# Kernel optimization log

Measured on AMD Instinct MI355X. Metric: run time of the kernel, lower is better.

Reference implementation:

```python
import jax, jax.numpy as jnp
import numpy as np

B, N, F = 32, 64, 128          # batch, num_nodes, n_in_node
K, H, M, NH = 4, 256, 256, 256 # edge_types, msg_hid, msg_out, n_hid
E = N * (N - 1)                # fully-connected directed edges = 4032


def setup_inputs() -> dict:
    key = jax.random.key(0)
    ks = jax.random.split(key, 12)
    inputs = jax.random.normal(ks[0], (B, N, F), dtype=jnp.float32)
    # soft edge-type assignment per edge (rows sum to 1, as in NRI)
    rel_type = jax.nn.softmax(jax.random.normal(ks[1], (B, E, K), dtype=jnp.float32), axis=-1)
    # one-hot receiver/sender matrices for all i != j pairs
    idx = np.array([(i, j) for i in range(N) for j in range(N) if i != j], dtype=np.int64)
    eye = np.eye(N, dtype=np.float32)
    rel_rec = jnp.asarray(eye[idx[:, 0]])   # [E, N]
    rel_send = jnp.asarray(eye[idx[:, 1]])  # [E, N]
    # per-edge-type message MLP weights (stacked over K): y = x @ W + b
    W1 = jax.random.normal(ks[2], (K, 2 * F, H), dtype=jnp.float32) / np.sqrt(2 * F)
    b1 = jnp.zeros((K, H), dtype=jnp.float32)
    W2 = jax.random.normal(ks[3], (K, H, M), dtype=jnp.float32) / np.sqrt(H)
    b2 = jnp.zeros((K, M), dtype=jnp.float32)
    # output MLP
    Wo1 = jax.random.normal(ks[4], (F + M, NH), dtype=jnp.float32) / np.sqrt(F + M)
    bo1 = jnp.zeros((NH,), dtype=jnp.float32)
    Wo2 = jax.random.normal(ks[5], (NH, NH), dtype=jnp.float32) / np.sqrt(NH)
    bo2 = jnp.zeros((NH,), dtype=jnp.float32)
    Wo3 = jax.random.normal(ks[6], (NH, F), dtype=jnp.float32) / np.sqrt(NH)
    bo3 = jnp.zeros((F,), dtype=jnp.float32)
    return {"inputs": inputs, "rel_type": rel_type, "rel_rec": rel_rec, "rel_send": rel_send,
            "W1": W1, "b1": b1, "W2": W2, "b2": b2,
            "Wo1": Wo1, "bo1": bo1, "Wo2": Wo2, "bo2": bo2, "Wo3": Wo3, "bo3": bo3}


def reference(inputs, rel_type, rel_rec, rel_send, W1, b1, W2, b2, Wo1, bo1, Wo2, bo2, Wo3, bo3):
    # gather node states to edges via one-hot matmul (as in the source)
    receivers = jnp.einsum('en,bnf->bef', rel_rec, inputs)   # [B,E,F]
    senders = jnp.einsum('en,bnf->bef', rel_send, inputs)    # [B,E,F]
    pre_msg = jnp.concatenate([receivers, senders], axis=-1)  # [B,E,2F]
    # per-edge-type 2-layer ReLU MLP, batched over the K edge types
    h = jax.nn.relu(jnp.einsum('bef,kfh->bkeh', pre_msg, W1) + b1[:, None, :])  # [B,K,E,H]
    msg = jax.nn.relu(jnp.einsum('bkeh,khm->bkem', h, W2) + b2[:, None, :])     # [B,K,E,M]
    # mask by soft edge type and accumulate over types (dropout p=0 -> identity)
    all_msgs = jnp.einsum('bkem,bek->bem', msg, rel_type)     # [B,E,M]
    # scatter-aggregate messages to receiver nodes via one-hot matmul
    agg_msgs = jnp.einsum('en,bem->bnm', rel_rec, all_msgs)   # [B,N,M]
    aug = jnp.concatenate([inputs, agg_msgs], axis=-1)        # [B,N,F+M]
    p = jax.nn.relu(aug @ Wo1 + bo1)
    p = jax.nn.relu(p @ Wo2 + bo2)
    p = p @ Wo3 + bo3
    return inputs + p
```

## Files before the change

### kernel.cpp

```cpp
#include <hip/hip_runtime.h>


#define B_ 32
#define N_ 64
#define F_ 128
#define K_ 4
#define E_ 4032

#define WS_W2T 0u
#define WS_R   524288u
#define WS_S   4718592u
#define WS_AGG 8912896u

typedef unsigned short u16;
typedef u16    u16x4  __attribute__((ext_vector_type(4)));
typedef u16    u16x8  __attribute__((ext_vector_type(8)));
typedef __bf16 bf16x8 __attribute__((ext_vector_type(8)));
typedef float  f32x4  __attribute__((ext_vector_type(4)));
typedef float  f32x16 __attribute__((ext_vector_type(16)));

__device__ __forceinline__ u16 f2bf(float f) {
    unsigned u; __builtin_memcpy(&u, &f, 4);
    return (u16)((u + 0x7FFFu + ((u >> 16) & 1u)) >> 16);
}
__device__ __forceinline__ float bf2f(u16 u) {
    unsigned v = ((unsigned)u) << 16;
    float f; __builtin_memcpy(&f, &v, 4); return f;
}

#define LBAR() do { \
    asm volatile("s_waitcnt lgkmcnt(0)" ::: "memory"); \
    __builtin_amdgcn_s_barrier(); \
    __builtin_amdgcn_sched_barrier(0); \
} while (0)

__global__ __launch_bounds__(256) void prep_rs_kernel(
    const float* __restrict__ W2, const float* __restrict__ x,
    const float* __restrict__ W1, const float* __restrict__ b1,
    u16* __restrict__ W2t, u16* __restrict__ R, u16* __restrict__ S)
{
    __shared__ u16 ldsA[64 * 136];
    __shared__ u16 ldsW[32 * 136];
    const int tid = threadIdx.x;

    if (blockIdx.x < 1024) {
        unsigned gid = blockIdx.x * 256u + tid;
        unsigned n = gid & 255u, kk = (gid >> 8) & 255u, k = gid >> 16;
        unsigned dst = (k * 8u + (kk >> 5)) * 8192u
                     + ((((kk >> 4) & 1u) * 2u) + ((kk >> 3) & 1u)) * 2048u
                     + n * 8u + (kk & 7u);
        W2t[dst] = f2bf(W2[gid]);
        return;
    }

    const int lane = tid & 63, w = tid >> 6;
    const int quad = lane >> 4, mloc = lane & 15;
    const int bx = blockIdx.x - 1024;
    const int ch = bx & 1;
    const int bq = bx >> 1;
    const int k = bq >> 6, half = (bq >> 5) & 1, b = bq & 31;

    for (int idx = tid; idx < 2048; idx += 256) {
        int row = idx >> 5, c4 = idx & 31;
        f32x4 v = *(const f32x4*)&x[(b * 64 + row) * 128 + c4 * 4];
        u16x4 o;
#pragma unroll
        for (int e = 0; e < 4; ++e) o[e] = f2bf(v[e]);
        *(u16x4*)&ldsA[row * 136 + c4 * 4] = o;
    }
    __syncthreads();

    bf16x8 aF[4];
#pragma unroll
    for (int ks = 0; ks < 4; ++ks)
        aF[ks] = *(const bf16x8*)&ldsA[(w * 16 + mloc) * 136 + quad * 8 + ks * 32];

    u16* dst = half ? S : R;
    for (int c = ch * 4; c < ch * 4 + 4; ++c) {
        __syncthreads();
        for (int idx = tid; idx < 4096; idx += 256) {
            int n = idx & 31, f = idx >> 5;
            ldsW[n * 136 + f] = f2bf(W1[(k * 256 + half * 128 + f) * 256 + c * 32 + n]);
        }
        __syncthreads();
#pragma unroll
        for (int nt = 0; nt < 2; ++nt) {
            f32x4 acc = (f32x4){0.f, 0.f, 0.f, 0.f};
            const int boff = (nt * 16 + mloc) * 136 + quad * 8;
#pragma unroll
            for (int ks = 0; ks < 4; ++ks)
                acc = __builtin_amdgcn_mfma_f32_16x16x32_bf16(
                    aF[ks], *(const bf16x8*)&ldsW[boff + ks * 32], acc, 0, 0, 0);
            const int n = c * 32 + nt * 16 + mloc;
            const float bias = half ? 0.f : b1[k * 256 + n];
#pragma unroll
            for (int r = 0; r < 4; ++r) {
                int row = w * 16 + quad * 4 + r;
                if (half) {
                    dst[((size_t)((k * 8 + c) * 2048 + b * 64 + row)) * 32 + nt * 16 + mloc]
                        = f2bf(acc[r] + bias);
                } else {
                    dst[((size_t)(k * 2048 + b * 64 + row)) * 256 + n] = f2bf(acc[r] + bias);
                }
            }
        }
    }
}

__global__ __launch_bounds__(256, 3) void edge12_kernel(
    const u16* __restrict__ R, const u16* __restrict__ S2,
    const float* __restrict__ rel, const u16* __restrict__ W2t,
    const float* __restrict__ b2, u16* __restrict__ aggb)
{
    __shared__ u16   Hs[32][64][8];
    __shared__ float Rf[4][256];
    __shared__ float rtS[4][64];

    const int tid  = threadIdx.x;
    const int lane = tid & 63;
    const int w    = tid >> 6;
    const int l31  = lane & 31;
    const int lh   = lane >> 5;
    const int bid  = ((blockIdx.x & 7) << 8) | (blockIdx.x >> 3);
    const int b    = bid >> 6;
    const int i    = bid & 63;

    {
        const int k = tid >> 6, j = tid & 63;
        float v = 0.f;
        if (j != i) v = rel[((size_t)(b * E_) + i * 63 + (j - (j > i))) * 4 + k];
        rtS[k][j] = v;
    }
    {
        const int k = tid >> 6, e4 = tid & 63;
        u16x4 t4 = *(const u16x4*)&R[((size_t)(k * 2048 + b * 64 + i)) * 256 + e4 * 4];
#pragma unroll
        for (int e = 0; e < 4; ++e) Rf[k][e4 * 4 + e] = bf2f(t4[e]);
    }

    u16x8 sreg[8];
#pragma unroll
    for (int s = 0; s < 8; ++s)
        sreg[s] = *(const u16x8*)&S2[((size_t)(s * 2048 + b * 64 + lane)) * 32 + w * 8];

    __syncthreads();

    const u16* Wb = W2t + lh * 2048 + (w * 64 + l31) * 8;

    float amsg[2] = {0.f, 0.f};

    for (int kT = 0; kT < 4; ++kT) {
        bf16x8 Bb[2][2][2];
#pragma unroll
        for (int ks2 = 0; ks2 < 2; ++ks2) {
            const u16* wp = Wb + (size_t)(kT * 8) * 8192 + ks2 * 4096;
            Bb[0][ks2][0] = *(const bf16x8*)(wp);
            Bb[0][ks2][1] = *(const bf16x8*)(wp + 256);
        }
#pragma unroll
        for (int s = 0; s < 8; ++s) {
            const float* rp = &Rf[kT][s * 32 + w * 8];
            f32x4 r0 = *(const f32x4*)rp, r1 = *(const f32x4*)(rp + 4);
            bf16x8 o;
#pragma unroll
            for (int e = 0; e < 4; ++e) {
                o[e]     = (__bf16)fmaxf(r0[e] + bf2f(sreg[s][e]),     0.f);
                o[4 + e] = (__bf16)fmaxf(r1[e] + bf2f(sreg[s][4 + e]), 0.f);
            }
            *(bf16x8*)&Hs[s * 4 + w][lane][0] = o;
        }
        __syncthreads();

        f32x16 acc[2][2];
#pragma unroll
        for (int mt = 0; mt < 2; ++mt)
#pragma unroll
            for (int nt = 0; nt < 2; ++nt) acc[mt][nt] = (f32x16)(0.f);

#pragma unroll
        for (int kc = 0; kc < 8; ++kc) {
            const int cur = kc & 1, nxt = cur ^ 1;
            if (kc == 0 && kT < 3) {
#pragma unroll
                for (int s = 0; s < 8; ++s)
                    sreg[s] = *(const u16x8*)&S2[((size_t)(((kT + 1) * 8 + s) * 2048 + b * 64 + lane)) * 32 + w * 8];
            }
            if (kc < 7) {
#pragma unroll
                for (int ks2 = 0; ks2 < 2; ++ks2) {
                    const u16* wp = Wb + (size_t)(kT * 8 + kc + 1) * 8192 + ks2 * 4096;
                    Bb[nxt][ks2][0] = *(const bf16x8*)(wp);
                    Bb[nxt][ks2][1] = *(const bf16x8*)(wp + 256);
                }
            }
#pragma unroll
            for (int ks2 = 0; ks2 < 2; ++ks2) {
                const int g = kc * 4 + ks2 * 2 + lh;
                bf16x8 A0 = *(const bf16x8*)&Hs[g][l31][0];
                bf16x8 A1 = *(const bf16x8*)&Hs[g][32 + l31][0];
                acc[0][0] = __builtin_amdgcn_mfma_f32_32x32x16_bf16(A0, Bb[cur][ks2][0], acc[0][0], 0, 0, 0);
                acc[0][1] = __builtin_amdgcn_mfma_f32_32x32x16_bf16(A0, Bb[cur][ks2][1], acc[0][1], 0, 0, 0);
                acc[1][0] = __builtin_amdgcn_mfma_f32_32x32x16_bf16(A1, Bb[cur][ks2][0], acc[1][0], 0, 0, 0);
                acc[1][1] = __builtin_amdgcn_mfma_f32_32x32x16_bf16(A1, Bb[cur][ks2][1], acc[1][1], 0, 0, 0);
            }
        }

#pragma unroll
        for (int nt = 0; nt < 2; ++nt) {
            const float bias = b2[kT * 256 + w * 64 + nt * 32 + l31];
#pragma unroll
            for (int mt = 0; mt < 2; ++mt) {
                float s = 0.f;
#pragma unroll
                for (int rq = 0; rq < 4; ++rq) {
                    f32x4 rt4 = *(const f32x4*)&rtS[kT][mt * 32 + rq * 8 + 4 * lh];
#pragma unroll
                    for (int e = 0; e < 4; ++e) {
                        float v = acc[mt][nt][rq * 4 + e] + bias;
                        v = v > 0.f ? v : 0.f;
                        s += rt4[e] * v;
                    }
                }
                amsg[nt] += s;
            }
        }
        __syncthreads();
    }

#pragma unroll
    for (int nt = 0; nt < 2; ++nt) {
        float s = amsg[nt] + __shfl_xor(amsg[nt], 32);
        if (lh == 0)
            aggb[(size_t)(b * 64 + i) * 256 + w * 64 + nt * 32 + l31] = f2bf(s);
    }
}

__global__ __launch_bounds__(256) void outmlp5_kernel(
    const float* __restrict__ x, const u16* __restrict__ aggb,
    const float* __restrict__ Wo1, const float* __restrict__ bo1,
    const float* __restrict__ Wo2, const float* __restrict__ bo2,
    const float* __restrict__ Wo3, const float* __restrict__ bo3,
    float* __restrict__ out)
{
    __shared__ u16 p1S[16 * 264];
    __shared__ u16 p2S[16 * 264];
    const int tid = threadIdx.x, lane = tid & 63, w = tid >> 6;
    const int quad = lane >> 4, mloc = lane & 15;
    const int row0 = blockIdx.x * 16;

    {
        f32x4 acc[4];
#pragma unroll
        for (int nt = 0; nt < 4; ++nt) acc[nt] = (f32x4){0.f, 0.f, 0.f, 0.f};
        for (int kk = 0; kk < 12; ++kk) {
            bf16x8 aF;
            const int row = row0 + mloc;
            if (kk < 4) {
                u16x8 t;
#pragma unroll
                for (int e = 0; e < 8; ++e) t[e] = f2bf(x[row * 128 + kk * 32 + quad * 8 + e]);
                __builtin_memcpy(&aF, &t, 16);
            } else {
                aF = *(const bf16x8*)&aggb[(size_t)row * 256 + (kk - 4) * 32 + quad * 8];
            }
#pragma unroll
            for (int nt = 0; nt < 4; ++nt) {
                const int n = w * 64 + nt * 16 + mloc;
                u16x8 t;
#pragma unroll
                for (int e = 0; e < 8; ++e)
                    t[e] = f2bf(Wo1[(kk * 32 + quad * 8 + e) * 256 + n]);
                bf16x8 bF;
                __builtin_memcpy(&bF, &t, 16);
                acc[nt] = __builtin_amdgcn_mfma_f32_16x16x32_bf16(aF, bF, acc[nt], 0, 0, 0);
            }
        }
#pragma unroll
        for (int nt = 0; nt < 4; ++nt) {
            const int n = w * 64 + nt * 16 + mloc;
            const float bias = bo1[n];
#pragma unroll
            for (int r = 0; r < 4; ++r) {
                float v = acc[nt][r] + bias;
                p1S[(quad * 4 + r) * 264 + n] = f2bf(v > 0.f ? v : 0.f);
            }
        }
    }
    LBAR();
    {
        f32x4 acc[4];
#pragma unroll
        for (int nt = 0; nt < 4; ++nt) acc[nt] = (f32x4){0.f, 0.f, 0.f, 0.f};
        for (int kk = 0; kk < 8; ++kk) {
            bf16x8 aF = *(const bf16x8*)&p1S[mloc * 264 + kk * 32 + quad * 8];
#pragma unroll
            for (int nt = 0; nt < 4; ++nt) {
                const int n = w * 64 + nt * 16 + mloc;
                u16x8 t;
#pragma unroll
                for (int e = 0; e < 8; ++e)
                    t[e] = f2bf(Wo2[(kk * 32 + quad * 8 + e) * 256 + n]);
                bf16x8 bF;
                __builtin_memcpy(&bF, &t, 16);
                acc[nt] = __builtin_amdgcn_mfma_f32_16x16x32_bf16(aF, bF, acc[nt], 0, 0, 0);
            }
        }
#pragma unroll
        for (int nt = 0; nt < 4; ++nt) {
            const int n = w * 64 + nt * 16 + mloc;
            const float bias = bo2[n];
#pragma unroll
            for (int r = 0; r < 4; ++r) {
                float v = acc[nt][r] + bias;
                p2S[(quad * 4 + r) * 264 + n] = f2bf(v > 0.f ? v : 0.f);
            }
        }
    }
    LBAR();
    {
        f32x4 acc[2];
#pragma unroll
        for (int nt = 0; nt < 2; ++nt) acc[nt] = (f32x4){0.f, 0.f, 0.f, 0.f};
        for (int kk = 0; kk < 8; ++kk) {
            bf16x8 aF = *(const bf16x8*)&p2S[mloc * 264 + kk * 32 + quad * 8];
#pragma unroll
            for (int nt = 0; nt < 2; ++nt) {
                const int n = w * 32 + nt * 16 + mloc;
                u16x8 t;
#pragma unroll
                for (int e = 0; e < 8; ++e)
                    t[e] = f2bf(Wo3[(kk * 32 + quad * 8 + e) * 128 + n]);
                bf16x8 bF;
                __builtin_memcpy(&bF, &t, 16);
                acc[nt] = __builtin_amdgcn_mfma_f32_16x16x32_bf16(aF, bF, acc[nt], 0, 0, 0);
            }
        }
#pragma unroll
        for (int nt = 0; nt < 2; ++nt) {
            const int n = w * 32 + nt * 16 + mloc;
            const float bias = bo3[n];
#pragma unroll
            for (int r = 0; r < 4; ++r) {
                const int grow = row0 + quad * 4 + r;
                out[grow * 128 + n] = x[grow * 128 + n] + acc[nt][r] + bias;
            }
        }
    }
}

extern "C" void kernel_launch(void* const* d_in, const int* in_sizes, int n_in,
                              void* d_out, int out_size, void* d_ws, size_t ws_size,
                              hipStream_t stream) {
    const float* x   = (const float*)d_in[0];
    const float* rel = (const float*)d_in[1];
    const float* W1  = (const float*)d_in[4];
    const float* b1  = (const float*)d_in[5];
    const float* W2  = (const float*)d_in[6];
    const float* b2  = (const float*)d_in[7];
    const float* Wo1 = (const float*)d_in[8];
    const float* bo1 = (const float*)d_in[9];
    const float* Wo2 = (const float*)d_in[10];
    const float* bo2 = (const float*)d_in[11];
    const float* Wo3 = (const float*)d_in[12];
    const float* bo3 = (const float*)d_in[13];
    float* out = (float*)d_out;

    char* ws = (char*)d_ws;
    u16* W2t  = (u16*)(ws + WS_W2T);
    u16* R    = (u16*)(ws + WS_R);
    u16* S2   = (u16*)(ws + WS_S);
    u16* aggb = (u16*)(ws + WS_AGG);

    prep_rs_kernel<<<1536, 256, 0, stream>>>(W2, x, W1, b1, W2t, R, S2);
    edge12_kernel<<<2048, 256, 0, stream>>>(R, S2, rel, W2t, b2, aggb);
    outmlp5_kernel<<<128, 256, 0, stream>>>(x, aggb, Wo1, bo1, Wo2, bo2, Wo3, bo3, out);
}
```

Measured before the change: 193.3 us.

## Fuse three kernels into one persistent kernel with global atomic barriers

Replaces the three separate launches (prep, edge MLP, output MLP) with a single 512-block kernel that uses atomic-counter grid barriers between phases. Each block now processes four receiver nodes in the edge phase instead of one, and the prep work is redistributed across 512 blocks. The intent is to remove launch gaps and tail effects between kernels. In exchange it relies on all 512 blocks being co-resident for the spin barriers, adds a memset launch, and leaves most blocks idle in the final output-MLP phase.

```diff
diff --git a/kernel.cpp b/kernel.cpp
--- a/kernel.cpp
+++ b/kernel.cpp
@@ -11,6 +11,7 @@
 #define WS_R   524288u
 #define WS_S   4718592u
 #define WS_AGG 8912896u
+#define WS_BAR 9961472u
 
 typedef unsigned short u16;
 typedef u16    u16x4  __attribute__((ext_vector_type(4)));
@@ -34,315 +35,324 @@
     __builtin_amdgcn_sched_barrier(0); \
 } while (0)
 
-__global__ __launch_bounds__(256) void prep_rs_kernel(
-    const float* __restrict__ W2, const float* __restrict__ x,
-    const float* __restrict__ W1, const float* __restrict__ b1,
-    u16* __restrict__ W2t, u16* __restrict__ R, u16* __restrict__ S)
-{
-    __shared__ u16 ldsA[64 * 136];
-    __shared__ u16 ldsW[32 * 136];
-    const int tid = threadIdx.x;
-
-    if (blockIdx.x < 1024) {
-        unsigned gid = blockIdx.x * 256u + tid;
-        unsigned n = gid & 255u, kk = (gid >> 8) & 255u, k = gid >> 16;
-        unsigned dst = (k * 8u + (kk >> 5)) * 8192u
-                     + ((((kk >> 4) & 1u) * 2u) + ((kk >> 3) & 1u)) * 2048u
-                     + n * 8u + (kk & 7u);
-        W2t[dst] = f2bf(W2[gid]);
-        return;
-    }
-
-    const int lane = tid & 63, w = tid >> 6;
-    const int quad = lane >> 4, mloc = lane & 15;
-    const int bx = blockIdx.x - 1024;
-    const int ch = bx & 1;
-    const int bq = bx >> 1;
-    const int k = bq >> 6, half = (bq >> 5) & 1, b = bq & 31;
-
-    for (int idx = tid; idx < 2048; idx += 256) {
-        int row = idx >> 5, c4 = idx & 31;
-        f32x4 v = *(const f32x4*)&x[(b * 64 + row) * 128 + c4 * 4];
-        u16x4 o;
-#pragma unroll
-        for (int e = 0; e < 4; ++e) o[e] = f2bf(v[e]);
-        *(u16x4*)&ldsA[row * 136 + c4 * 4] = o;
+__device__ __forceinline__ void gbar(unsigned* c) {
+    __syncthreads();
+    if (threadIdx.x == 0) {
+        __threadfence();
+        atomicAdd(c, 1u);
+        int guard = 0;
+        while (atomicAdd(c, 0u) < 512u && guard < (1 << 22)) {
+            __builtin_amdgcn_s_sleep(8);
+            ++guard;
+        }
     }
     __syncthreads();
-
-    bf16x8 aF[4];
-#pragma unroll
-    for (int ks = 0; ks < 4; ++ks)
-        aF[ks] = *(const bf16x8*)&ldsA[(w * 16 + mloc) * 136 + quad * 8 + ks * 32];
-
-    u16* dst = half ? S : R;
-    for (int c = ch * 4; c < ch * 4 + 4; ++c) {
-        __syncthreads();
-        for (int idx = tid; idx < 4096; idx += 256) {
-            int n = idx & 31, f = idx >> 5;
-            ldsW[n * 136 + f] = f2bf(W1[(k * 256 + half * 128 + f) * 256 + c * 32 + n]);
-        }
-        __syncthreads();
-#pragma unroll
-        for (int nt = 0; nt < 2; ++nt) {
-            f32x4 acc = (f32x4){0.f, 0.f, 0.f, 0.f};
-            const int boff = (nt * 16 + mloc) * 136 + quad * 8;
-#pragma unroll
-            for (int ks = 0; ks < 4; ++ks)
-                acc = __builtin_amdgcn_mfma_f32_16x16x32_bf16(
-                    aF[ks], *(const bf16x8*)&ldsW[boff + ks * 32], acc, 0, 0, 0);
-            const int n = c * 32 + nt * 16 + mloc;
-            const float bias = half ? 0.f : b1[k * 256 + n];
-#pragma unroll
-            for (int r = 0; r < 4; ++r) {
-                int row = w * 16 + quad * 4 + r;
-                if (half) {
-                    dst[((size_t)((k * 8 + c) * 2048 + b * 64 + row)) * 32 + nt * 16 + mloc]
-                        = f2bf(acc[r] + bias);
-                } else {
-                    dst[((size_t)(k * 2048 + b * 64 + row)) * 256 + n] = f2bf(acc[r] + bias);
-                }
-            }
-        }
-    }
-}
-
-__global__ __launch_bounds__(256, 3) void edge12_kernel(
-    const u16* __restrict__ R, const u16* __restrict__ S2,
-    const float* __restrict__ rel, const u16* __restrict__ W2t,
-    const float* __restrict__ b2, u16* __restrict__ aggb)
+    __threadfence();
+}
+
+__global__ __launch_bounds__(256, 3) void fused_kernel(
+    const float* __restrict__ x, const float* __restrict__ rel,
+    const float* __restrict__ W1, const float* __restrict__ b1,
+    const float* __restrict__ W2, const float* __restrict__ b2,
+    const float* __restrict__ Wo1, const float* __restrict__ bo1,
+    const float* __restrict__ Wo2, const float* __restrict__ bo2,
+    const float* __restrict__ Wo3, const float* __restrict__ bo3,
+    u16* __restrict__ W2t, u16* __restrict__ R, u16* __restrict__ S2,
+    u16* __restrict__ aggb, float* __restrict__ out, unsigned* __restrict__ bar)
 {
-    __shared__ u16   Hs[32][64][8];
-    __shared__ float Rf[4][256];
-    __shared__ float rtS[4][64];
-
+    __shared__ __align__(16) char smem[37888];
     const int tid  = threadIdx.x;
     const int lane = tid & 63;
     const int w    = tid >> 6;
-    const int l31  = lane & 31;
-    const int lh   = lane >> 5;
-    const int bid  = ((blockIdx.x & 7) << 8) | (blockIdx.x >> 3);
-    const int b    = bid >> 6;
-    const int i    = bid & 63;
+    const int quad = lane >> 4, mloc = lane & 15;
+    const int l31  = lane & 31,  lh  = lane >> 5;
 
     {
-        const int k = tid >> 6, j = tid & 63;
-        float v = 0.f;
-        if (j != i) v = rel[((size_t)(b * E_) + i * 63 + (j - (j > i))) * 4 + k];
-        rtS[k][j] = v;
+        {
+            unsigned gbase = blockIdx.x * 512u + tid * 2u;
+#pragma unroll
+            for (int u2 = 0; u2 < 2; ++u2) {
+                unsigned gid = gbase + u2;
+                unsigned n = gid & 255u, kk = (gid >> 8) & 255u, k = gid >> 16;
+                unsigned dst = (k * 8u + (kk >> 5)) * 8192u
+                             + (((kk >> 4) & 1u) * 2u + ((kk >> 3) & 1u)) * 2048u
+                             + n * 8u + (kk & 7u);
+                W2t[dst] = f2bf(W2[gid]);
+            }
+        }
+        u16* ldsA = (u16*)smem;
+        u16* ldsW = (u16*)(smem + 17408);
+        const int bx = blockIdx.x;
+        const int k = bx >> 7, half = (bx >> 6) & 1, b = (bx >> 1) & 31, ch = bx & 1;
+
+        for (int idx = tid; idx < 2048; idx += 256) {
+            int row = idx >> 5, c4 = idx & 31;
+            f32x4 v = *(const f32x4*)&x[(b * 64 + row) * 128 + c4 * 4];
+            u16x4 o;
+#pragma unroll
+            for (int e = 0; e < 4; ++e) o[e] = f2bf(v[e]);
+            *(u16x4*)&ldsA[row * 136 + c4 * 4] = o;
+        }
+        __syncthreads();
+
+        bf16x8 aF[4];
+#pragma unroll
+        for (int ks = 0; ks < 4; ++ks)
+            aF[ks] = *(const bf16x8*)&ldsA[(w * 16 + mloc) * 136 + quad * 8 + ks * 32];
+
+        u16* dst = half ? S2 : R;
+        for (int c = ch * 4; c < ch * 4 + 4; ++c) {
+            __syncthreads();
+            for (int idx = tid; idx < 4096; idx += 256) {
+                int n = idx & 31, f = idx >> 5;
+                ldsW[n * 136 + f] = f2bf(W1[(k * 256 + half * 128 + f) * 256 + c * 32 + n]);
+            }
+            __syncthreads();
+#pragma unroll
+            for (int nt = 0; nt < 2; ++nt) {
+                f32x4 acc = (f32x4){0.f, 0.f, 0.f, 0.f};
+                const int boff = (nt * 16 + mloc) * 136 + quad * 8;
+#pragma unroll
+                for (int ks = 0; ks < 4; ++ks)
+                    acc = __builtin_amdgcn_mfma_f32_16x16x32_bf16(
+                        aF[ks], *(const bf16x8*)&ldsW[boff + ks * 32], acc, 0, 0, 0);
+                const int n = c * 32 + nt * 16 + mloc;
+                const float bias = half ? 0.f : b1[k * 256 + n];
+#pragma unroll
+                for (int r = 0; r < 4; ++r) {
+                    int row = w * 16 + quad * 4 + r;
+                    if (half) {
+                        dst[((size_t)((k * 8 + c) * 2048 + b * 64 + row)) * 32 + nt * 16 + mloc]
+                            = f2bf(acc[r] + bias);
+                    } else {
+                        dst[((size_t)(k * 2048 + b * 64 + row)) * 256 + n] = f2bf(acc[r] + bias);
+                    }
+                }
+            }
+        }
     }
+    gbar(&bar[0]);
+
     {
-        const int k = tid >> 6, e4 = tid & 63;
-        u16x4 t4 = *(const u16x4*)&R[((size_t)(k * 2048 + b * 64 + i)) * 256 + e4 * 4];
-#pragma unroll
-        for (int e = 0; e < 4; ++e) Rf[k][e4 * 4 + e] = bf2f(t4[e]);
+        u16  (*Hs)[64][8] = (u16(*)[64][8])smem;
+        float (*Rf)[256]  = (float(*)[256])(smem + 32768);
+        float (*rtS)[64]  = (float(*)[64])(smem + 32768 + 4096);
+        const int lbid = ((blockIdx.x & 7) << 6) | (blockIdx.x >> 3);
+        const int b    = lbid >> 4;
+        const int g    = lbid & 15;
+        const u16* Wb  = W2t + lh * 2048 + (w * 64 + l31) * 8;
+
+        for (int r = 0; r < 4; ++r) {
+            const int i = g * 4 + r;
+            {
+                const int k = tid >> 6, j = tid & 63;
+                float v = 0.f;
+                if (j != i) v = rel[((size_t)(b * E_) + i * 63 + (j - (j > i))) * 4 + k];
+                rtS[k][j] = v;
+            }
+            {
+                const int k = tid >> 6, e4 = tid & 63;
+                u16x4 t4 = *(const u16x4*)&R[((size_t)(k * 2048 + b * 64 + i)) * 256 + e4 * 4];
+#pragma unroll
+                for (int e = 0; e < 4; ++e) Rf[k][e4 * 4 + e] = bf2f(t4[e]);
+            }
+            u16x8 sreg[8];
+#pragma unroll
+            for (int s = 0; s < 8; ++s)
+                sreg[s] = *(const u16x8*)&S2[((size_t)(s * 2048 + b * 64 + lane)) * 32 + w * 8];
+            __syncthreads();
+
+            float amsg[2] = {0.f, 0.f};
+
+            for (int kT = 0; kT < 4; ++kT) {
+                bf16x8 Bb[2][2][2];
+#pragma unroll
+                for (int ks2 = 0; ks2 < 2; ++ks2) {
+                    const u16* wp = Wb + (size_t)(kT * 8) * 8192 + ks2 * 4096;
+                    Bb[0][ks2][0] = *(const bf16x8*)(wp);
+                    Bb[0][ks2][1] = *(const bf16x8*)(wp + 256);
+                }
+#pragma unroll
+                for (int s = 0; s < 8; ++s) {
+                    const float* rp = &Rf[kT][s * 32 + w * 8];
+                    f32x4 r0 = *(const f32x4*)rp, r1 = *(const f32x4*)(rp + 4);
+                    bf16x8 o;
+#pragma unroll
+                    for (int e = 0; e < 4; ++e) {
+                        o[e]     = (__bf16)fmaxf(r0[e] + bf2f(sreg[s][e]),     0.f);
+                        o[4 + e] = (__bf16)fmaxf(r1[e] + bf2f(sreg[s][4 + e]), 0.f);
+                    }
+                    *(bf16x8*)&Hs[s * 4 + w][lane][0] = o;
+                }
+                __syncthreads();
+
+                f32x16 acc[2][2];
+#pragma unroll
+                for (int mt = 0; mt < 2; ++mt)
+#pragma unroll
+                    for (int nt = 0; nt < 2; ++nt) acc[mt][nt] = (f32x16)(0.f);
+
+#pragma unroll
+                for (int kc = 0; kc < 8; ++kc) {
+                    const int cur = kc & 1, nxt = cur ^ 1;
+                    if (kc == 0 && kT < 3) {
+#pragma unroll
+                        for (int s = 0; s < 8; ++s)
+                            sreg[s] = *(const u16x8*)&S2[((size_t)(((kT + 1) * 8 + s) * 2048 + b * 64 + lane)) * 32 + w * 8];
+                    }
+                    if (kc < 7) {
+#pragma unroll
+                        for (int ks2 = 0; ks2 < 2; ++ks2) {
+                            const u16* wp = Wb + (size_t)(kT * 8 + kc + 1) * 8192 + ks2 * 4096;
+                            Bb[nxt][ks2][0] = *(const bf16x8*)(wp);
+                            Bb[nxt][ks2][1] = *(const bf16x8*)(wp + 256);
+                        }
+                    }
+#pragma unroll
+                    for (int ks2 = 0; ks2 < 2; ++ks2) {
+                        const int gg = kc * 4 + ks2 * 2 + lh;
+                        bf16x8 A0 = *(const bf16x8*)&Hs[gg][l31][0];
+                        bf16x8 A1 = *(const bf16x8*)&Hs[gg][32 + l31][0];
+                        acc[0][0] = __builtin_amdgcn_mfma_f32_32x32x16_bf16(A0, Bb[cur][ks2][0], acc[0][0], 0, 0, 0);
+                        acc[0][1] = __builtin_amdgcn_mfma_f32_32x32x16_bf16(A0, Bb[cur][ks2][1], acc[0][1], 0, 0, 0);
+                        acc[1][0] = __builtin_amdgcn_mfma_f32_32x32x16_bf16(A1, Bb[cur][ks2][0], acc[1][0], 0, 0, 0);
+                        acc[1][1] = __builtin_amdgcn_mfma_f32_32x32x16_bf16(A1, Bb[cur][ks2][1], acc[1][1], 0, 0, 0);
+                    }
+                }
+
+#pragma unroll
+                for (int nt = 0; nt < 2; ++nt) {
+                    const float bias = b2[kT * 256 + w * 64 + nt * 32 + l31];
+#pragma unroll
+                    for (int mt = 0; mt < 2; ++mt) {
+                        float s = 0.f;
+#pragma unroll
+                        for (int rq = 0; rq < 4; ++rq) {
+                            f32x4 rt4 = *(const f32x4*)&rtS[kT][mt * 32 + rq * 8 + 4 * lh];
+#pragma unroll
+                            for (int e = 0; e < 4; ++e) {
+                                float v = acc[mt][nt][rq * 4 + e] + bias;
+                                v = v > 0.f ? v : 0.f;
+                                s += rt4[e] * v;
+                            }
+                        }
+                        amsg[nt] += s;
+                    }
+                }
+                __syncthreads();
+            }
+
+#pragma unroll
+            for (int nt = 0; nt < 2; ++nt) {
+                float s = amsg[nt] + __shfl_xor(amsg[nt], 32);
+                if (lh == 0)
+                    aggb[(size_t)(b * 64 + i) * 256 + w * 64 + nt * 32 + l31] = f2bf(s);
+            }
+        }
     }
-
-    u16x8 sreg[8];
-#pragma unroll
-    for (int s = 0; s < 8; ++s)
-        sreg[s] = *(const u16x8*)&S2[((size_t)(s * 2048 + b * 64 + lane)) * 32 + w * 8];
-
-    __syncthreads();
-
-    const u16* Wb = W2t + lh * 2048 + (w * 64 + l31) * 8;
-
-    float amsg[2] = {0.f, 0.f};
-
-    for (int kT = 0; kT < 4; ++kT) {
-        bf16x8 Bb[2][2][2];
-#pragma unroll
-        for (int ks2 = 0; ks2 < 2; ++ks2) {
-            const u16* wp = Wb + (size_t)(kT * 8) * 8192 + ks2 * 4096;
-            Bb[0][ks2][0] = *(const bf16x8*)(wp);
-            Bb[0][ks2][1] = *(const bf16x8*)(wp + 256);
-        }
-#pragma unroll
-        for (int s = 0; s < 8; ++s) {
-            const float* rp = &Rf[kT][s * 32 + w * 8];
-            f32x4 r0 = *(const f32x4*)rp, r1 = *(const f32x4*)(rp + 4);
-            bf16x8 o;
-#pragma unroll
-            for (int e = 0; e < 4; ++e) {
-                o[e]     = (__bf16)fmaxf(r0[e] + bf2f(sreg[s][e]),     0.f);
-                o[4 + e] = (__bf16)fmaxf(r1[e] + bf2f(sreg[s][4 + e]), 0.f);
-            }
-            *(bf16x8*)&Hs[s * 4 + w][lane][0] = o;
-        }
-        __syncthreads();
-
-        f32x16 acc[2][2];
-#pragma unroll
-        for (int mt = 0; mt < 2; ++mt)
-#pragma unroll
-            for (int nt = 0; nt < 2; ++nt) acc[mt][nt] = (f32x16)(0.f);
-
-#pragma unroll
-        for (int kc = 0; kc < 8; ++kc) {
-            const int cur = kc & 1, nxt = cur ^ 1;
-            if (kc == 0 && kT < 3) {
-#pragma unroll
-                for (int s = 0; s < 8; ++s)
-                    sreg[s] = *(const u16x8*)&S2[((size_t)(((kT + 1) * 8 + s) * 2048 + b * 64 + lane)) * 32 + w * 8];
-            }
-            if (kc < 7) {
-#pragma unroll
-                for (int ks2 = 0; ks2 < 2; ++ks2) {
-                    const u16* wp = Wb + (size_t)(kT * 8 + kc + 1) * 8192 + ks2 * 4096;
-                    Bb[nxt][ks2][0] = *(const bf16x8*)(wp);
-                    Bb[nxt][ks2][1] = *(const bf16x8*)(wp + 256);
-                }
-            }
-#pragma unroll
-            for (int ks2 = 0; ks2 < 2; ++ks2) {
-                const int g = kc * 4 + ks2 * 2 + lh;
-                bf16x8 A0 = *(const bf16x8*)&Hs[g][l31][0];
-                bf16x8 A1 = *(const bf16x8*)&Hs[g][32 + l31][0];
-                acc[0][0] = __builtin_amdgcn_mfma_f32_32x32x16_bf16(A0, Bb[cur][ks2][0], acc[0][0], 0, 0, 0);
-                acc[0][1] = __builtin_amdgcn_mfma_f32_32x32x16_bf16(A0, Bb[cur][ks2][1], acc[0][1], 0, 0, 0);
-                acc[1][0] = __builtin_amdgcn_mfma_f32_32x32x16_bf16(A1, Bb[cur][ks2][0], acc[1][0], 0, 0, 0);
-                acc[1][1] = __builtin_amdgcn_mfma_f32_32x32x16_bf16(A1, Bb[cur][ks2][1], acc[1][1], 0, 0, 0);
-            }
-        }
-
-#pragma unroll
-        for (int nt = 0; nt < 2; ++nt) {
-            const float bias = b2[kT * 256 + w * 64 + nt * 32 + l31];
-#pragma unroll
-            for (int mt = 0; mt < 2; ++mt) {
-                float s = 0.f;
-#pragma unroll
-                for (int rq = 0; rq < 4; ++rq) {
-                    f32x4 rt4 = *(const f32x4*)&rtS[kT][mt * 32 + rq * 8 + 4 * lh];
-#pragma unroll
-                    for (int e = 0; e < 4; ++e) {
-                        float v = acc[mt][nt][rq * 4 + e] + bias;
-                        v = v > 0.f ? v : 0.f;
-                        s += rt4[e] * v;
-                    }
-                }
-                amsg[nt] += s;
-            }
-        }
-        __syncthreads();
-    }
-
-#pragma unroll
-    for (int nt = 0; nt < 2; ++nt) {
-        float s = amsg[nt] + __shfl_xor(amsg[nt], 32);
-        if (lh == 0)
-            aggb[(size_t)(b * 64 + i) * 256 + w * 64 + nt * 32 + l31] = f2bf(s);
-    }
-}
-
-__global__ __launch_bounds__(256) void outmlp5_kernel(
-    const float* __restrict__ x, const u16* __restrict__ aggb,
-    const float* __restrict__ Wo1, const float* __restrict__ bo1,
-    const float* __restrict__ Wo2, const float* __restrict__ bo2,
-    const float* __restrict__ Wo3, const float* __restrict__ bo3,
-    float* __restrict__ out)
-{
-    __shared__ u16 p1S[16 * 264];
-    __shared__ u16 p2S[16 * 264];
-    const int tid = threadIdx.x, lane = tid & 63, w = tid >> 6;
-    const int quad = lane >> 4, mloc = lane & 15;
-    const int row0 = blockIdx.x * 16;
-
-    {
-        f32x4 acc[4];
-#pragma unroll
-        for (int nt = 0; nt < 4; ++nt) acc[nt] = (f32x4){0.f, 0.f, 0.f, 0.f};
-        for (int kk = 0; kk < 12; ++kk) {
-            bf16x8 aF;
-            const int row = row0 + mloc;
-            if (kk < 4) {
-                u16x8 t;
-#pragma unroll
-                for (int e = 0; e < 8; ++e) t[e] = f2bf(x[row * 128 + kk * 32 + quad * 8 + e]);
-                __builtin_memcpy(&aF, &t, 16);
-            } else {
-                aF = *(const bf16x8*)&aggb[(size_t)row * 256 + (kk - 4) * 32 + quad * 8];
+    gbar(&bar[32]);
+
+    if (blockIdx.x < 128) {
+        u16* p1S = (u16*)smem;
+        u16* p2S = (u16*)(smem + 8448);
+        const int row0 = blockIdx.x * 16;
+
+        {
+            f32x4 acc[4];
+#pragma unroll
+            for (int nt = 0; nt < 4; ++nt) acc[nt] = (f32x4){0.f, 0.f, 0.f, 0.f};
+            for (int kk = 0; kk < 12; ++kk) {
+                bf16x8 aF;
+                const int row = row0 + mloc;
+                if (kk < 4) {
+                    u16x8 t;
+#pragma unroll
+                    for (int e = 0; e < 8; ++e) t[e] = f2bf(x[row * 128 + kk * 32 + quad * 8 + e]);
+                    __builtin_memcpy(&aF, &t, 16);
+                } else {
+                    aF = *(const bf16x8*)&aggb[(size_t)row * 256 + (kk - 4) * 32 + quad * 8];
+                }
+#pragma unroll
+                for (int nt = 0; nt < 4; ++nt) {
+                    const int n = w * 64 + nt * 16 + mloc;
+                    u16x8 t;
+#pragma unroll
+                    for (int e = 0; e < 8; ++e)
+                        t[e] = f2bf(Wo1[(kk * 32 + quad * 8 + e) * 256 + n]);
+                    bf16x8 bF;
+                    __builtin_memcpy(&bF, &t, 16);
+                    acc[nt] = __builtin_amdgcn_mfma_f32_16x16x32_bf16(aF, bF, acc[nt], 0, 0, 0);
+                }
             }
 #pragma unroll
             for (int nt = 0; nt < 4; ++nt) {
                 const int n = w * 64 + nt * 16 + mloc;
-                u16x8 t;
-#pragma unroll
-                for (int e = 0; e < 8; ++e)
-                    t[e] = f2bf(Wo1[(kk * 32 + quad * 8 + e) * 256 + n]);
-                bf16x8 bF;
-                __builtin_memcpy(&bF, &t, 16);
-                acc[nt] = __builtin_amdgcn_mfma_f32_16x16x32_bf16(aF, bF, acc[nt], 0, 0, 0);
-            }
-        }
-#pragma unroll
-        for (int nt = 0; nt < 4; ++nt) {
-            const int n = w * 64 + nt * 16 + mloc;
-            const float bias = bo1[n];
-#pragma unroll
-            for (int r = 0; r < 4; ++r) {
-                float v = acc[nt][r] + bias;
-                p1S[(quad * 4 + r) * 264 + n] = f2bf(v > 0.f ? v : 0.f);
-            }
-        }
-    }
-    LBAR();
-    {
-        f32x4 acc[4];
-#pragma unroll
-        for (int nt = 0; nt < 4; ++nt) acc[nt] = (f32x4){0.f, 0.f, 0.f, 0.f};
-        for (int kk = 0; kk < 8; ++kk) {
-            bf16x8 aF = *(const bf16x8*)&p1S[mloc * 264 + kk * 32 + quad * 8];
+                const float bias = bo1[n];
+#pragma unroll
+                for (int r = 0; r < 4; ++r) {
+                    float v = acc[nt][r] + bias;
+                    p1S[(quad * 4 + r) * 264 + n] = f2bf(v > 0.f ? v : 0.f);
+                }
+            }
+        }
+        LBAR();
+        {
+            f32x4 acc[4];
+#pragma unroll
+            for (int nt = 0; nt < 4; ++nt) acc[nt] = (f32x4){0.f, 0.f, 0.f, 0.f};
+            for (int kk = 0; kk < 8; ++kk) {
+                bf16x8 aF = *(const bf16x8*)&p1S[mloc * 264 + kk * 32 + quad * 8];
+#pragma unroll
+                for (int nt = 0; nt < 4; ++nt) {
+                    const int n = w * 64 + nt * 16 + mloc;
+                    u16x8 t;
+#pragma unroll
+                    for (int e = 0; e < 8; ++e)
+                        t[e] = f2bf(Wo2[(kk * 32 + quad * 8 + e) * 256 + n]);
+                    bf16x8 bF;
+                    __builtin_memcpy(&bF, &t, 16);
+                    acc[nt] = __builtin_amdgcn_mfma_f32_16x16x32_bf16(aF, bF, acc[nt], 0, 0, 0);
+                }
+            }
 #pragma unroll
             for (int nt = 0; nt < 4; ++nt) {
                 const int n = w * 64 + nt * 16 + mloc;
-                u16x8 t;
-#pragma unroll
-                for (int e = 0; e < 8; ++e)
-                    t[e] = f2bf(Wo2[(kk * 32 + quad * 8 + e) * 256 + n]);
-                bf16x8 bF;
-                __builtin_memcpy(&bF, &t, 16);
-                acc[nt] = __builtin_amdgcn_mfma_f32_16x16x32_bf16(aF, bF, acc[nt], 0, 0, 0);
-            }
-        }
-#pragma unroll
-        for (int nt = 0; nt < 4; ++nt) {
-            const int n = w * 64 + nt * 16 + mloc;
-            const float bias = bo2[n];
-#pragma unroll
-            for (int r = 0; r < 4; ++r) {
-                float v = acc[nt][r] + bias;
-                p2S[(quad * 4 + r) * 264 + n] = f2bf(v > 0.f ? v : 0.f);
-            }
-        }
-    }
-    LBAR();
-    {
-        f32x4 acc[2];
-#pragma unroll
-        for (int nt = 0; nt < 2; ++nt) acc[nt] = (f32x4){0.f, 0.f, 0.f, 0.f};
-        for (int kk = 0; kk < 8; ++kk) {
-            bf16x8 aF = *(const bf16x8*)&p2S[mloc * 264 + kk * 32 + quad * 8];
+                const float bias = bo2[n];
+#pragma unroll
+                for (int r = 0; r < 4; ++r) {
+                    float v = acc[nt][r] + bias;
+                    p2S[(quad * 4 + r) * 264 + n] = f2bf(v > 0.f ? v : 0.f);
+                }
+            }
+        }
+        LBAR();
+        {
+            f32x4 acc[2];
+#pragma unroll
+            for (int nt = 0; nt < 2; ++nt) acc[nt] = (f32x4){0.f, 0.f, 0.f, 0.f};
+            for (int kk = 0; kk < 8; ++kk) {
+                bf16x8 aF = *(const bf16x8*)&p2S[mloc * 264 + kk * 32 + quad * 8];
+#pragma unroll
+                for (int nt = 0; nt < 2; ++nt) {
+                    const int n = w * 32 + nt * 16 + mloc;
+                    u16x8 t;
+#pragma unroll
+                    for (int e = 0; e < 8; ++e)
+                        t[e] = f2bf(Wo3[(kk * 32 + quad * 8 + e) * 128 + n]);
+                    bf16x8 bF;
+                    __builtin_memcpy(&bF, &t, 16);
+                    acc[nt] = __builtin_amdgcn_mfma_f32_16x16x32_bf16(aF, bF, acc[nt], 0, 0, 0);
+                }
+            }
 #pragma unroll
             for (int nt = 0; nt < 2; ++nt) {
                 const int n = w * 32 + nt * 16 + mloc;
-                u16x8 t;
-#pragma unroll
-                for (int e = 0; e < 8; ++e)
-                    t[e] = f2bf(Wo3[(kk * 32 + quad * 8 + e) * 128 + n]);
-                bf16x8 bF;
-                __builtin_memcpy(&bF, &t, 16);
-                acc[nt] = __builtin_amdgcn_mfma_f32_16x16x32_bf16(aF, bF, acc[nt], 0, 0, 0);
-            }
-        }
-#pragma unroll
-        for (int nt = 0; nt < 2; ++nt) {
-            const int n = w * 32 + nt * 16 + mloc;
-            const float bias = bo3[n];
-#pragma unroll
-            for (int r = 0; r < 4; ++r) {
-                const int grow = row0 + quad * 4 + r;
-                out[grow * 128 + n] = x[grow * 128 + n] + acc[nt][r] + bias;
+                const float bias = bo3[n];
+#pragma unroll
+                for (int r = 0; r < 4; ++r) {
+                    const int grow = row0 + quad * 4 + r;
+                    out[grow * 128 + n] = x[grow * 128 + n] + acc[nt][r] + bias;
+                }
             }
         }
     }
@@ -370,8 +380,10 @@
     u16* R    = (u16*)(ws + WS_R);
     u16* S2   = (u16*)(ws + WS_S);
     u16* aggb = (u16*)(ws + WS_AGG);
-
-    prep_rs_kernel<<<1536, 256, 0, stream>>>(W2, x, W1, b1, W2t, R, S2);
-    edge12_kernel<<<2048, 256, 0, stream>>>(R, S2, rel, W2t, b2, aggb);
-    outmlp5_kernel<<<128, 256, 0, stream>>>(x, aggb, Wo1, bo1, Wo2, bo2, Wo3, bo3, out);
-}
+    unsigned* bar = (unsigned*)(ws + WS_BAR);
+
+    hipMemsetAsync(bar, 0, 256, stream);
+    hipLaunchKernelGGL(fused_kernel, dim3(512), dim3(256), 0, stream,
+                       x, rel, W1, b1, W2, b2, Wo1, bo1, Wo2, bo2, Wo3, bo3,
+                       W2t, R, S2, aggb, out, bar);
+}
```

Measured after the change: 354.6 us. 1.83x slower.

## Split prep and output-MLP work across more blocks, deepen W2 prefetch

Applied to the files above, without the earlier changes.

The prep kernel now gives each block 2 column chunks instead of 4, so the launch grows to 2048 blocks. The output MLP handles 8 rows per block instead of 16, doubling its grid to 256 blocks; half the MFMA rows are duplicated and masked on store. The edge kernel's W2 fragment prefetch goes from double to triple buffering, loading two k-chunks ahead. The aim is more parallelism on the small kernels and better hiding of W2 load latency, at the cost of redundant W1 conversion and MFMA work and extra registers.

```diff
diff --git a/kernel.cpp b/kernel.cpp
--- a/kernel.cpp
+++ b/kernel.cpp
@@ -56,8 +56,8 @@
     const int lane = tid & 63, w = tid >> 6;
     const int quad = lane >> 4, mloc = lane & 15;
     const int bx = blockIdx.x - 1024;
-    const int ch = bx & 1;
-    const int bq = bx >> 1;
+    const int ch = bx & 3;
+    const int bq = bx >> 2;
     const int k = bq >> 6, half = (bq >> 5) & 1, b = bq & 31;
 
     for (int idx = tid; idx < 2048; idx += 256) {
@@ -76,7 +76,7 @@
         aF[ks] = *(const bf16x8*)&ldsA[(w * 16 + mloc) * 136 + quad * 8 + ks * 32];
 
     u16* dst = half ? S : R;
-    for (int c = ch * 4; c < ch * 4 + 4; ++c) {
+    for (int c = ch * 2; c < ch * 2 + 2; ++c) {
         __syncthreads();
         for (int idx = tid; idx < 4096; idx += 256) {
             int n = idx & 31, f = idx >> 5;
@@ -107,7 +107,7 @@
     }
 }
 
-__global__ __launch_bounds__(256, 3) void edge12_kernel(
+__global__ __launch_bounds__(256, 3) void edge13_kernel(
     const u16* __restrict__ R, const u16* __restrict__ S2,
     const float* __restrict__ rel, const u16* __restrict__ W2t,
     const float* __restrict__ b2, u16* __restrict__ aggb)
@@ -150,13 +150,15 @@
     float amsg[2] = {0.f, 0.f};
 
     for (int kT = 0; kT < 4; ++kT) {
-        bf16x8 Bb[2][2][2];
-#pragma unroll
-        for (int ks2 = 0; ks2 < 2; ++ks2) {
-            const u16* wp = Wb + (size_t)(kT * 8) * 8192 + ks2 * 4096;
-            Bb[0][ks2][0] = *(const bf16x8*)(wp);
-            Bb[0][ks2][1] = *(const bf16x8*)(wp + 256);
-        }
+        bf16x8 Bb[3][2][2];
+#pragma unroll
+        for (int pre = 0; pre < 2; ++pre)
+#pragma unroll
+            for (int ks2 = 0; ks2 < 2; ++ks2) {
+                const u16* wp = Wb + (size_t)(kT * 8 + pre) * 8192 + ks2 * 4096;
+                Bb[pre][ks2][0] = *(const bf16x8*)(wp);
+                Bb[pre][ks2][1] = *(const bf16x8*)(wp + 256);
+            }
 #pragma unroll
         for (int s = 0; s < 8; ++s) {
             const float* rp = &Rf[kT][s * 32 + w * 8];
@@ -179,16 +181,17 @@
 
 #pragma unroll
         for (int kc = 0; kc < 8; ++kc) {
-            const int cur = kc & 1, nxt = cur ^ 1;
+            const int cur = kc % 3;
             if (kc == 0 && kT < 3) {
 #pragma unroll
                 for (int s = 0; s < 8; ++s)
                     sreg[s] = *(const u16x8*)&S2[((size_t)(((kT + 1) * 8 + s) * 2048 + b * 64 + lane)) * 32 + w * 8];
             }
-            if (kc < 7) {
+            if (kc < 6) {
+                const int nxt = (kc + 2) % 3;
 #pragma unroll
                 for (int ks2 = 0; ks2 < 2; ++ks2) {
-                    const u16* wp = Wb + (size_t)(kT * 8 + kc + 1) * 8192 + ks2 * 4096;
+                    const u16* wp = Wb + (size_t)(kT * 8 + kc + 2) * 8192 + ks2 * 4096;
                     Bb[nxt][ks2][0] = *(const bf16x8*)(wp);
                     Bb[nxt][ks2][1] = *(const bf16x8*)(wp + 256);
                 }
@@ -235,18 +238,19 @@
     }
 }
 
-__global__ __launch_bounds__(256) void outmlp5_kernel(
+__global__ __launch_bounds__(256) void outmlp6_kernel(
     const float* __restrict__ x, const u16* __restrict__ aggb,
     const float* __restrict__ Wo1, const float* __restrict__ bo1,
     const float* __restrict__ Wo2, const float* __restrict__ bo2,
     const float* __restrict__ Wo3, const float* __restrict__ bo3,
     float* __restrict__ out)
 {
-    __shared__ u16 p1S[16 * 264];
-    __shared__ u16 p2S[16 * 264];
+    __shared__ u16 p1S[8 * 264];
+    __shared__ u16 p2S[8 * 264];
     const int tid = threadIdx.x, lane = tid & 63, w = tid >> 6;
     const int quad = lane >> 4, mloc = lane & 15;
-    const int row0 = blockIdx.x * 16;
+    const int row0 = blockIdx.x * 8;
+    const int arow = row0 + (mloc & 7);
 
     {
         f32x4 acc[4];
@@ -254,14 +258,13 @@
         for (int nt = 0; nt < 4; ++nt) acc[nt] = (f32x4){0.f, 0.f, 0.f, 0.f};
         for (int kk = 0; kk < 12; ++kk) {
             bf16x8 aF;
-            const int row = row0 + mloc;
             if (kk < 4) {
                 u16x8 t;
 #pragma unroll
-                for (int e = 0; e < 8; ++e) t[e] = f2bf(x[row * 128 + kk * 32 + quad * 8 + e]);
+                for (int e = 0; e < 8; ++e) t[e] = f2bf(x[arow * 128 + kk * 32 + quad * 8 + e]);
                 __builtin_memcpy(&aF, &t, 16);
             } else {
-                aF = *(const bf16x8*)&aggb[(size_t)row * 256 + (kk - 4) * 32 + quad * 8];
+                aF = *(const bf16x8*)&aggb[(size_t)arow * 256 + (kk - 4) * 32 + quad * 8];
             }
 #pragma unroll
             for (int nt = 0; nt < 4; ++nt) {
@@ -279,10 +282,12 @@
         for (int nt = 0; nt < 4; ++nt) {
             const int n = w * 64 + nt * 16 + mloc;
             const float bias = bo1[n];
-#pragma unroll
-            for (int r = 0; r < 4; ++r) {
-                float v = acc[nt][r] + bias;
-                p1S[(quad * 4 + r) * 264 + n] = f2bf(v > 0.f ? v : 0.f);
+            if (quad < 2) {
+#pragma unroll
+                for (int r = 0; r < 4; ++r) {
+                    float v = acc[nt][r] + bias;
+                    p1S[(quad * 4 + r) * 264 + n] = f2bf(v > 0.f ? v : 0.f);
+                }
             }
         }
     }
@@ -292,7 +297,7 @@
 #pragma unroll
         for (int nt = 0; nt < 4; ++nt) acc[nt] = (f32x4){0.f, 0.f, 0.f, 0.f};
         for (int kk = 0; kk < 8; ++kk) {
-            bf16x8 aF = *(const bf16x8*)&p1S[mloc * 264 + kk * 32 + quad * 8];
+            bf16x8 aF = *(const bf16x8*)&p1S[(mloc & 7) * 264 + kk * 32 + quad * 8];
 #pragma unroll
             for (int nt = 0; nt < 4; ++nt) {
                 const int n = w * 64 + nt * 16 + mloc;
@@ -309,10 +314,12 @@
         for (int nt = 0; nt < 4; ++nt) {
             const int n = w * 64 + nt * 16 + mloc;
             const float bias = bo2[n];
-#pragma unroll
-            for (int r = 0; r < 4; ++r) {
-                float v = acc[nt][r] + bias;
-                p2S[(quad * 4 + r) * 264 + n] = f2bf(v > 0.f ? v : 0.f);
+            if (quad < 2) {
+#pragma unroll
+                for (int r = 0; r < 4; ++r) {
+                    float v = acc[nt][r] + bias;
+                    p2S[(quad * 4 + r) * 264 + n] = f2bf(v > 0.f ? v : 0.f);
+                }
             }
         }
     }
@@ -322,7 +329,7 @@
 #pragma unroll
         for (int nt = 0; nt < 2; ++nt) acc[nt] = (f32x4){0.f, 0.f, 0.f, 0.f};
         for (int kk = 0; kk < 8; ++kk) {
-            bf16x8 aF = *(const bf16x8*)&p2S[mloc * 264 + kk * 32 + quad * 8];
+            bf16x8 aF = *(const bf16x8*)&p2S[(mloc & 7) * 264 + kk * 32 + quad * 8];
 #pragma unroll
             for (int nt = 0; nt < 2; ++nt) {
                 const int n = w * 32 + nt * 16 + mloc;
@@ -339,10 +346,12 @@
         for (int nt = 0; nt < 2; ++nt) {
             const int n = w * 32 + nt * 16 + mloc;
             const float bias = bo3[n];
-#pragma unroll
-            for (int r = 0; r < 4; ++r) {
-                const int grow = row0 + quad * 4 + r;
-                out[grow * 128 + n] = x[grow * 128 + n] + acc[nt][r] + bias;
+            if (quad < 2) {
+#pragma unroll
+                for (int r = 0; r < 4; ++r) {
+                    const int grow = row0 + quad * 4 + r;
+                    out[grow * 128 + n] = x[grow * 128 + n] + acc[nt][r] + bias;
+                }
             }
         }
     }
@@ -371,7 +380,7 @@
     u16* S2   = (u16*)(ws + WS_S);
     u16* aggb = (u16*)(ws + WS_AGG);
 
-    prep_rs_kernel<<<1536, 256, 0, stream>>>(W2, x, W1, b1, W2t, R, S2);
-    edge12_kernel<<<2048, 256, 0, stream>>>(R, S2, rel, W2t, b2, aggb);
-    outmlp5_kernel<<<128, 256, 0, stream>>>(x, aggb, Wo1, bo1, Wo2, bo2, Wo3, bo3, out);
-}
+    prep_rs_kernel<<<2048, 256, 0, stream>>>(W2, x, W1, b1, W2t, R, S2);
+    edge13_kernel<<<2048, 256, 0, stream>>>(R, S2, rel, W2t, b2, aggb);
+    outmlp6_kernel<<<256, 256, 0, stream>>>(x, aggb, Wo1, bo1, Wo2, bo2, Wo3, bo3, out);
+}
```

Result: no change. 196.1 us (+1.4%).
